# Performance work log

Measured on AMD Instinct MI355X. Metric: run time of the kernel, lower is better.

Reference implementation:

```python
import jax, jax.numpy as jnp
import numpy as np
import math

UNIT = 46
KEY_SIZE = 16
MAX_POS = 50
NEG_BIG = 1.0e12


def _rope_tables(max_pos, d):
    pos = np.arange(max_pos, dtype=np.float32)[:, None]
    div = np.exp(np.arange(0, d, 2, dtype=np.float32) * (-math.log(10000.0) / d))
    sin = np.sin(pos * div)  # [P, d/2]
    cos = np.cos(pos * div)  # [P, d/2]
    # matches torch repeat_interleave(2, dim=-1) of the strided sinusoid table
    cos_rep = np.repeat(cos, 2, axis=-1)  # [P, d]
    sin_rep = np.repeat(sin, 2, axis=-1)  # [P, d]
    return jnp.asarray(cos_rep), jnp.asarray(sin_rep)

_COS, _SIN = _rope_tables(MAX_POS, KEY_SIZE)


def _apply_rope(qw):
    # qw: [B, S, d]
    s = qw.shape[-2]
    qw2 = jnp.stack([-qw[..., 1::2], qw[..., ::2]], axis=-1).reshape(qw.shape)
    return qw * _COS[:s] + qw2 * _SIN[:s]


def setup_inputs() -> dict:
    key = jax.random.key(0)
    ks = jax.random.split(key, 8)
    B, S = 32768, 50
    x = jax.random.normal(ks[0], (B, S, UNIT), dtype=jnp.float32)
    mask = jnp.ones((B, S), dtype=jnp.float32)
    d_in = UNIT
    sc = 1.0 / math.sqrt(d_in)
    Wi = jax.random.uniform(ks[1], (2 * UNIT + KEY_SIZE, d_in), minval=-sc, maxval=sc, dtype=jnp.float32)
    bi = jax.random.uniform(ks[2], (2 * UNIT + KEY_SIZE,), minval=-sc, maxval=sc, dtype=jnp.float32)
    Wo = jax.random.uniform(ks[3], (UNIT, UNIT), minval=-sc, maxval=sc, dtype=jnp.float32)
    bo = jax.random.uniform(ks[4], (UNIT,), minval=-sc, maxval=sc, dtype=jnp.float32)
    Wq = jax.random.uniform(ks[5], (1, UNIT), minval=-sc, maxval=sc, dtype=jnp.float32)
    bq = jax.random.uniform(ks[6], (1,), minval=-sc, maxval=sc, dtype=jnp.float32)
    scale_q = jnp.ones((KEY_SIZE,), jnp.float32)
    offset_q = jnp.zeros((KEY_SIZE,), jnp.float32)
    scale_k = jnp.ones((KEY_SIZE,), jnp.float32)
    offset_k = jnp.zeros((KEY_SIZE,), jnp.float32)
    return {"x": x, "mask": mask, "Wi": Wi, "bi": bi, "Wo": Wo, "bo": bo,
            "scale_q": scale_q, "offset_q": offset_q, "scale_k": scale_k,
            "offset_k": offset_k, "Wq": Wq, "bq": bq}


def reference(x, mask, Wi, bi, Wo, bo, scale_q, offset_q, scale_k, offset_k, Wq, bq):
    # x: [B, S, U], mask: [B, S]
    h = jax.nn.silu(jnp.einsum('bsu,ou->bso', x, Wi) + bi)  # [B, S, 2U+K]
    u, v, qk = jnp.split(h, [UNIT, 2 * UNIT], axis=-1)
    q = _apply_rope(qk * scale_q + offset_q)  # [B, S, K]
    k = _apply_rope(qk * scale_k + offset_k)  # [B, S, K]
    A = jnp.einsum('bik,bjk->bij', q, k) / math.sqrt(KEY_SIZE)  # [B, S, S]
    m = mask[:, None, :]
    A = jax.nn.softmax(A * m + (1.0 - m) * (-NEG_BIG), axis=-1)
    # NOTE: original overwrites the gated output with a plain matmul (u unused)
    out = jnp.einsum('bij,bju->biu', A, v)  # [B, S, U]
    out = jnp.einsum('biu,ou->bio', out, Wo) + bo  # [B, S, U]
    prob = (jnp.einsum('bsu,ou->bso', out, Wq) + bq)[..., 0]  # [B, S]
    prob = prob * mask - (1.0 - mask) * NEG_BIG
    prob = jax.nn.softmax(prob, axis=-1)
    return jnp.sum(out * prob[..., None], axis=1)  # [B, U]
```

## Files before the change

kernel.cpp:

```cpp
#include <hip/hip_runtime.h>
#include <math.h>

#define SEQ 50
#define UNITD 46
#define NEGBIG 1000000000000.0f

typedef _Float16 f16;
typedef f16 f16x4 __attribute__((ext_vector_type(4)));
typedef f16 f16x8 __attribute__((ext_vector_type(8)));
typedef float f32x4 __attribute__((ext_vector_type(4)));

__device__ __forceinline__ float rcpf(float x) { return __builtin_amdgcn_rcpf(x); }

#define ARENA 12800
#define QOFF 0
#define KOFF 2560
#define VOFF 6400
#define MOFF 12544

__device__ __forceinline__ int swzP(int row, int colbyte) {
    return row * 128 + (colbyte ^ ((row & 7) << 4));
}
__device__ __forceinline__ int swzV(int row, int colbyte) {
    return VOFF + row * 128 + (colbyte ^ ((row & 7) << 4));
}

__global__ void prep_kernel(const float* __restrict__ Wi,
                            const float* __restrict__ Wo,
                            f16x8* __restrict__ ws)
{
    const int lane = threadIdx.x & 63;
    const int g = lane >> 4, t = lane & 15;
    #pragma unroll
    for (int nt = 0; nt < 4; ++nt) {
        int c = t + 16 * nt; bool cok = c < 62;
        const float* wr = Wi + (size_t)(UNITD + (cok ? c : 0)) * UNITD;
        #pragma unroll
        for (int kt = 0; kt < 2; ++kt) {
            f16x8 f;
            #pragma unroll
            for (int jj = 0; jj < 8; ++jj) {
                int u = 32 * kt + 8 * g + jj;
                f[jj] = (f16)((cok && u < UNITD) ? wr[u] : 0.f);
            }
            ws[(nt * 2 + kt) * 64 + lane] = f;
        }
    }
    #pragma unroll
    for (int mo = 0; mo < 3; ++mo) {
        int o = 16 * mo + t; bool ook = o < UNITD;
        const float* wr = Wo + (size_t)(ook ? o : 0) * UNITD;
        #pragma unroll
        for (int kt = 0; kt < 2; ++kt) {
            f16x8 f;
            #pragma unroll
            for (int jj = 0; jj < 8; ++jj) {
                int u = 32 * kt + 8 * g + jj;
                f[jj] = (f16)((ook && u < UNITD) ? wr[u] : 0.f);
            }
            ws[512 + (mo * 2 + kt) * 64 + lane] = f;
        }
    }
}

__global__ __launch_bounds__(256, 3) void gau_kernel(
    const float* __restrict__ x,
    const float* __restrict__ mask,
    const f16x8* __restrict__ wf,
    const float* __restrict__ bi,
    const float* __restrict__ bo,
    const float* __restrict__ sq,
    const float* __restrict__ oq,
    const float* __restrict__ sk,
    const float* __restrict__ ok,
    const float* __restrict__ Wq,
    const float* __restrict__ bq,
    float* __restrict__ out,
    int Btot)
{
    const int lane = threadIdx.x & 63;
    const int wid  = threadIdx.x >> 6;
    const int b    = blockIdx.x * 4 + wid;
    const int g    = lane >> 4;
    const int t    = lane & 15;

    __shared__ __align__(16) char smem[4 * ARENA];
    char* wa = smem + wid * ARENA;
    float* M = (float*)(wa + MOFF);

    if (b >= Btot) return;

    M[lane] = (lane < SEQ) ? mask[(size_t)b * SEQ + lane] : 0.f;

    f16x8 bfW[4][2];
    float biv[4];
    #pragma unroll
    for (int nt = 0; nt < 4; ++nt) {
        int c = t + 16 * nt;
        biv[nt] = (c < 62) ? bi[UNITD + c] : 0.f;
        #pragma unroll
        for (int kt = 0; kt < 2; ++kt)
            bfW[nt][kt] = wf[(nt * 2 + kt) * 64 + lane];
    }

    f32x4 hB[4][4];
    #pragma unroll
    for (int mt = 0; mt < 4; ++mt)
        #pragma unroll
        for (int nt = 0; nt < 4; ++nt) {
            f32x4 c; c[0] = biv[nt]; c[1] = biv[nt]; c[2] = biv[nt]; c[3] = biv[nt];
            hB[mt][nt] = c;
        }

    const float* xb = x + (size_t)b * (SEQ * UNITD);
    #pragma unroll
    for (int mt = 0; mt < 4; ++mt) {
        int row = 16 * mt + t; if (row > SEQ - 1) row = SEQ - 1;
        const float* xr = xb + row * UNITD;
        #pragma unroll
        for (int kt = 0; kt < 2; ++kt) {
            f16x8 ax;
            #pragma unroll
            for (int jj = 0; jj < 8; jj += 2) {
                int u = 32 * kt + 8 * g + jj;
                float lo = 0.f, hi = 0.f;
                if (u < UNITD) { float2 w = *(const float2*)(xr + u); lo = w.x; hi = w.y; }
                ax[jj] = (f16)lo; ax[jj + 1] = (f16)hi;
            }
            #pragma unroll
            for (int nt = 0; nt < 4; ++nt)
                hB[mt][nt] = __builtin_amdgcn_mfma_f32_16x16x32_f16(ax, bfW[nt][kt], hB[mt][nt], 0, 0, 0);
        }
    }

    float qkv[4][4];
    #pragma unroll
    for (int mt = 0; mt < 4; ++mt) {
        float s2[4], s3[4];
        #pragma unroll
        for (int nt = 0; nt < 4; ++nt) {
            float sl[4];
            #pragma unroll
            for (int r = 0; r < 4; ++r) {
                float h = hB[mt][nt][r];
                sl[r] = h * rcpf(1.f + __expf(-h));
            }
            int ucol = t + 16 * nt;
            if (nt < 3 && ucol < UNITD) {
                f16x4 pv;
                #pragma unroll
                for (int r = 0; r < 4; ++r) pv[r] = (f16)sl[r];
                *(f16x4*)(wa + swzV(ucol, (16 * mt + 4 * g) * 2)) = pv;
            }
            if (nt == 2) { s2[0]=sl[0]; s2[1]=sl[1]; s2[2]=sl[2]; s2[3]=sl[3]; }
            if (nt == 3) { s3[0]=sl[0]; s3[1]=sl[1]; s3[2]=sl[2]; s3[3]=sl[3]; }
        }
        #pragma unroll
        for (int r = 0; r < 4; ++r) qkv[mt][r] = (t >= 14) ? s2[r] : s3[r];
    }

    {
        f16* Q = (f16*)(wa + QOFF);
        f16* K = (f16*)(wa + KOFF);
        int d = (t >= 14) ? (t - 14) : (t + 2);
        float invf = __expf(-(float)(d >> 1) * 1.1512925464970229f);
        float sgn  = (d & 1) ? 1.f : -1.f;
        float sqd = sq[d], oqd = oq[d], skd = sk[d], okd = ok[d];
        #pragma unroll
        for (int mt = 0; mt < 4; ++mt)
            #pragma unroll
            for (int r = 0; r < 4; ++r) {
                int seq = 16 * mt + 4 * g + r;
                float qv = qkv[mt][r] * sqd + oqd;
                float kv = qkv[mt][r] * skd + okd;
                float qp = __shfl_xor(qv, 1);
                float kp = __shfl_xor(kv, 1);
                float sn, cs;
                __sincosf((float)seq * invf, &sn, &cs);
                Q[seq * 20 + d] = (f16)(qv * cs + sgn * qp * sn);
                K[seq * 20 + d] = (f16)(kv * cs + sgn * kp * sn);
            }
    }

    f16x4 ak[4], bq_[4];
    #pragma unroll
    for (int m4 = 0; m4 < 4; ++m4) ak[m4]  = *(f16x4*)(wa + KOFF + (16 * m4 + t) * 40 + 8 * g);
    #pragma unroll
    for (int n4 = 0; n4 < 4; ++n4) bq_[n4] = *(f16x4*)(wa + QOFF + (16 * n4 + t) * 40 + 8 * g);

    f32x4 pT[4][4];
    #pragma unroll
    for (int m4 = 0; m4 < 4; ++m4)
        #pragma unroll
        for (int n4 = 0; n4 < 4; ++n4) {
            f32x4 z; z[0]=0.f; z[1]=0.f; z[2]=0.f; z[3]=0.f;
            pT[m4][n4] = __builtin_amdgcn_mfma_f32_16x16x16f16(ak[m4], bq_[n4], z, 0, 0, 0);
        }

    float mjv[4][4];
    #pragma unroll
    for (int m4 = 0; m4 < 4; ++m4)
        #pragma unroll
        for (int r = 0; r < 4; ++r) mjv[m4][r] = M[16 * m4 + 4 * g + r];

    #pragma unroll
    for (int n4 = 0; n4 < 4; ++n4) {
        float a_[4][4]; float mx = -INFINITY;
        #pragma unroll
        for (int m4 = 0; m4 < 4; ++m4)
            #pragma unroll
            for (int r = 0; r < 4; ++r) {
                float mj = mjv[m4][r];
                float av = pT[m4][n4][r] * 0.25f * mj - (1.f - mj) * NEGBIG;
                a_[m4][r] = av; mx = fmaxf(mx, av);
            }
        mx = fmaxf(mx, __shfl_xor(mx, 16)); mx = fmaxf(mx, __shfl_xor(mx, 32));
        float sm = 0.f;
        #pragma unroll
        for (int m4 = 0; m4 < 4; ++m4)
            #pragma unroll
            for (int r = 0; r < 4; ++r) { float e = __expf(a_[m4][r] - mx); a_[m4][r] = e; sm += e; }
        sm += __shfl_xor(sm, 16); sm += __shfl_xor(sm, 32);
        float inv = rcpf(sm);
        int i = t + 16 * n4;
        if (i < SEQ) {
            #pragma unroll
            for (int m4 = 0; m4 < 4; ++m4) {
                f16x4 pk;
                #pragma unroll
                for (int r = 0; r < 4; ++r) pk[r] = (f16)(a_[m4][r] * inv);
                *(f16x4*)(wa + swzP(i, (16 * m4 + 4 * g) * 2)) = pk;
            }
        }
    }

    f16x8 bv[3][2];
    #pragma unroll
    for (int nt = 0; nt < 3; ++nt)
        #pragma unroll
        for (int kt = 0; kt < 2; ++kt)
            bv[nt][kt] = *(f16x8*)(wa + swzV(t + 16 * nt, (32 * kt + 8 * g) * 2));

    f32x4 oA[4][3];
    #pragma unroll
    for (int mt = 0; mt < 4; ++mt)
        #pragma unroll
        for (int nt = 0; nt < 3; ++nt) { f32x4 z; z[0]=0.f; z[1]=0.f; z[2]=0.f; z[3]=0.f; oA[mt][nt] = z; }

    #pragma unroll
    for (int mt = 0; mt < 4; ++mt) {
        int pr = 16 * mt + t; if (pr > SEQ - 1) pr = SEQ - 1;
        #pragma unroll
        for (int kt = 0; kt < 2; ++kt) {
            f16x8 ap = *(f16x8*)(wa + swzP(pr, (32 * kt + 8 * g) * 2));
            #pragma unroll
            for (int nt = 0; nt < 3; ++nt)
                oA[mt][nt] = __builtin_amdgcn_mfma_f32_16x16x32_f16(ap, bv[nt][kt], oA[mt][nt], 0, 0, 0);
        }
    }

    #pragma unroll
    for (int mt = 0; mt < 4; ++mt)
        #pragma unroll
        for (int nt = 0; nt < 3; ++nt) {
            int u = t + 16 * nt;
            if (u < UNITD) {
                #pragma unroll
                for (int r = 0; r < 4; ++r) {
                    int i = 4 * g + r + 16 * mt;
                    if (i < SEQ)
                        *(f16*)(wa + swzP(i, u * 2)) = (f16)oA[mt][nt][r];
                }
            }
        }

    f16x8 aw[3][2];
    #pragma unroll
    for (int mo = 0; mo < 3; ++mo)
        #pragma unroll
        for (int kt = 0; kt < 2; ++kt)
            aw[mo][kt] = wf[512 + (mo * 2 + kt) * 64 + lane];

    f32x4 o2[3][4];
    #pragma unroll
    for (int mo = 0; mo < 3; ++mo)
        #pragma unroll
        for (int n4 = 0; n4 < 4; ++n4) { f32x4 z; z[0]=0.f; z[1]=0.f; z[2]=0.f; z[3]=0.f; o2[mo][n4] = z; }

    #pragma unroll
    for (int n4 = 0; n4 < 4; ++n4) {
        int br = t + 16 * n4; if (br > SEQ - 1) br = SEQ - 1;
        #pragma unroll
        for (int kt = 0; kt < 2; ++kt) {
            f16x8 bo_ = *(f16x8*)(wa + swzP(br, (32 * kt + 8 * g) * 2));
            #pragma unroll
            for (int mo = 0; mo < 3; ++mo)
                o2[mo][n4] = __builtin_amdgcn_mfma_f32_16x16x32_f16(aw[mo][kt], bo_, o2[mo][n4], 0, 0, 0);
        }
    }

    float bov[3][4], wqv[3][4];
    #pragma unroll
    for (int mo = 0; mo < 3; ++mo)
        #pragma unroll
        for (int r = 0; r < 4; ++r) {
            int o = 16 * mo + 4 * g + r; bool ok2 = (o < UNITD);
            bov[mo][r] = ok2 ? bo[o] : 0.f;
            wqv[mo][r] = ok2 ? Wq[o] : 0.f;
        }
    #pragma unroll
    for (int mo = 0; mo < 3; ++mo)
        #pragma unroll
        for (int n4 = 0; n4 < 4; ++n4)
            #pragma unroll
            for (int r = 0; r < 4; ++r) o2[mo][n4][r] += bov[mo][r];

    float bq0 = bq[0];
    float tv[4]; float mx2 = -INFINITY;
    #pragma unroll
    for (int n4 = 0; n4 < 4; ++n4) {
        float s = 0.f;
        #pragma unroll
        for (int mo = 0; mo < 3; ++mo)
            #pragma unroll
            for (int r = 0; r < 4; ++r) s += o2[mo][n4][r] * wqv[mo][r];
        s += __shfl_xor(s, 16); s += __shfl_xor(s, 32);
        float hq = s + bq0;
        float mi = M[t + 16 * n4];
        tv[n4] = hq * mi - (1.f - mi) * NEGBIG;
        mx2 = fmaxf(mx2, tv[n4]);
    }
    #pragma unroll
    for (int off = 1; off <= 8; off <<= 1) mx2 = fmaxf(mx2, __shfl_xor(mx2, off));
    float sm2 = 0.f;
    #pragma unroll
    for (int n4 = 0; n4 < 4; ++n4) { float e = __expf(tv[n4] - mx2); tv[n4] = e; sm2 += e; }
    #pragma unroll
    for (int off = 1; off <= 8; off <<= 1) sm2 += __shfl_xor(sm2, off);
    float inv2 = rcpf(sm2);

    #pragma unroll
    for (int mo = 0; mo < 3; ++mo) {
        float racc[4];
        #pragma unroll
        for (int r = 0; r < 4; ++r) {
            float a = 0.f;
            #pragma unroll
            for (int n4 = 0; n4 < 4; ++n4) a += o2[mo][n4][r] * tv[n4];
            racc[r] = a;
        }
        #pragma unroll
        for (int off = 1; off <= 8; off <<= 1)
            #pragma unroll
            for (int r = 0; r < 4; ++r) racc[r] += __shfl_xor(racc[r], off);
        if (t == 0) {
            #pragma unroll
            for (int r = 0; r < 4; ++r) {
                int o = 16 * mo + 4 * g + r;
                if (o < UNITD) out[(size_t)b * UNITD + o] = racc[r] * inv2;
            }
        }
    }
}

extern "C" void kernel_launch(void* const* d_in, const int* in_sizes, int n_in,
                              void* d_out, int out_size, void* d_ws, size_t ws_size,
                              hipStream_t stream) {
    const float* x    = (const float*)d_in[0];
    const float* mask = (const float*)d_in[1];
    const float* Wi   = (const float*)d_in[2];
    const float* bi   = (const float*)d_in[3];
    const float* Wo   = (const float*)d_in[4];
    const float* bo   = (const float*)d_in[5];
    const float* sq   = (const float*)d_in[6];
    const float* oq   = (const float*)d_in[7];
    const float* sk   = (const float*)d_in[8];
    const float* ok   = (const float*)d_in[9];
    const float* Wq   = (const float*)d_in[10];
    const float* bq   = (const float*)d_in[11];
    float* outp       = (float*)d_out;

    prep_kernel<<<1, 64, 0, stream>>>(Wi, Wo, (f16x8*)d_ws);

    const int B = in_sizes[0] / (SEQ * UNITD);
    const int blocks = (B + 3) / 4;
    gau_kernel<<<blocks, 256, 0, stream>>>(x, mask, (const f16x8*)d_ws, bi, bo,
                                           sq, oq, sk, ok, Wq, bq, outp, B);
}
```

Baseline: 202.8 us.

## Shrink per-wave LDS arena with padded 104-byte row stride to raise occupancy

Replaces the 128-byte XOR-swizzled row layout for the P and V tiles with an unswizzled 104-byte row stride (52 halves). This shrinks the per-wave LDS arena from 12800 to 10240 bytes, and the launch bound is raised from 3 to 4 blocks per CU. Stores that would fall past the 50-sequence boundary are now skipped. The out-of-range K-columns in the V operand are masked to zero in registers, so the padding rows and columns never need to be zeroed. The aim is more resident waves to hide latency. The cost is possible LDS bank conflicts without the swizzle, plus register pressure from the tighter launch bound.

```diff
diff --git a/kernel.cpp b/kernel.cpp
--- a/kernel.cpp
+++ b/kernel.cpp
@@ -9,21 +9,16 @@
 typedef f16 f16x4 __attribute__((ext_vector_type(4)));
 typedef f16 f16x8 __attribute__((ext_vector_type(8)));
 typedef float f32x4 __attribute__((ext_vector_type(4)));
+typedef unsigned u32x4 __attribute__((ext_vector_type(4)));
 
 __device__ __forceinline__ float rcpf(float x) { return __builtin_amdgcn_rcpf(x); }
 
-#define ARENA 12800
+#define ARENA 10240
 #define QOFF 0
 #define KOFF 2560
-#define VOFF 6400
-#define MOFF 12544
-
-__device__ __forceinline__ int swzP(int row, int colbyte) {
-    return row * 128 + (colbyte ^ ((row & 7) << 4));
-}
-__device__ __forceinline__ int swzV(int row, int colbyte) {
-    return VOFF + row * 128 + (colbyte ^ ((row & 7) << 4));
-}
+#define VOFF 5200
+#define MOFF 9984
+#define PSTR 104
 
 __global__ void prep_kernel(const float* __restrict__ Wi,
                             const float* __restrict__ Wo,
@@ -63,7 +58,7 @@
     }
 }
 
-__global__ __launch_bounds__(256, 3) void gau_kernel(
+__global__ __launch_bounds__(256, 4) void gau_kernel(
     const float* __restrict__ x,
     const float* __restrict__ mask,
     const f16x8* __restrict__ wf,
@@ -146,11 +141,13 @@
                 sl[r] = h * rcpf(1.f + __expf(-h));
             }
             int ucol = t + 16 * nt;
-            if (nt < 3 && ucol < UNITD) {
+            if (nt < 3 && ucol < UNITD && (mt < 3 || g == 0)) {
+                int seqb = 16 * mt + 4 * g;
                 f16x4 pv;
                 #pragma unroll
-                for (int r = 0; r < 4; ++r) pv[r] = (f16)sl[r];
-                *(f16x4*)(wa + swzV(ucol, (16 * mt + 4 * g) * 2)) = pv;
+                for (int r = 0; r < 4; ++r)
+                    pv[r] = (seqb + r < SEQ) ? (f16)sl[r] : (f16)0.f;
+                *(f16x4*)(wa + VOFF + ucol * PSTR + seqb * 2) = pv;
             }
             if (nt == 2) { s2[0]=sl[0]; s2[1]=sl[1]; s2[2]=sl[2]; s2[3]=sl[3]; }
             if (nt == 3) { s3[0]=sl[0]; s3[1]=sl[1]; s3[2]=sl[2]; s3[3]=sl[3]; }
@@ -226,10 +223,11 @@
         if (i < SEQ) {
             #pragma unroll
             for (int m4 = 0; m4 < 4; ++m4) {
+                if (m4 == 3 && g != 0) continue;
                 f16x4 pk;
                 #pragma unroll
                 for (int r = 0; r < 4; ++r) pk[r] = (f16)(a_[m4][r] * inv);
-                *(f16x4*)(wa + swzP(i, (16 * m4 + 4 * g) * 2)) = pk;
+                *(f16x4*)(wa + i * PSTR + (16 * m4 + 4 * g) * 2) = pk;
             }
         }
     }
@@ -238,8 +236,17 @@
     #pragma unroll
     for (int nt = 0; nt < 3; ++nt)
         #pragma unroll
-        for (int kt = 0; kt < 2; ++kt)
-            bv[nt][kt] = *(f16x8*)(wa + swzV(t + 16 * nt, (32 * kt + 8 * g) * 2));
+        for (int kt = 0; kt < 2; ++kt) {
+            f16x8 v = *(f16x8*)(wa + VOFF + (t + 16 * nt) * PSTR + (32 * kt + 8 * g) * 2);
+            if (kt == 1) {
+                u32x4 w = __builtin_bit_cast(u32x4, v);
+                unsigned mlo = (g <= 2) ? 0xFFFFFFFFu : 0u;
+                unsigned mhi = (g <= 1) ? 0xFFFFFFFFu : 0u;
+                w[0] &= mlo; w[1] &= mlo; w[2] &= mhi; w[3] &= mhi;
+                v = __builtin_bit_cast(f16x8, w);
+            }
+            bv[nt][kt] = v;
+        }
 
     f32x4 oA[4][3];
     #pragma unroll
@@ -252,7 +259,7 @@
         int pr = 16 * mt + t; if (pr > SEQ - 1) pr = SEQ - 1;
         #pragma unroll
         for (int kt = 0; kt < 2; ++kt) {
-            f16x8 ap = *(f16x8*)(wa + swzP(pr, (32 * kt + 8 * g) * 2));
+            f16x8 ap = *(f16x8*)(wa + pr * PSTR + (32 * kt + 8 * g) * 2);
             #pragma unroll
             for (int nt = 0; nt < 3; ++nt)
                 oA[mt][nt] = __builtin_amdgcn_mfma_f32_16x16x32_f16(ap, bv[nt][kt], oA[mt][nt], 0, 0, 0);
@@ -269,7 +276,7 @@
                 for (int r = 0; r < 4; ++r) {
                     int i = 4 * g + r + 16 * mt;
                     if (i < SEQ)
-                        *(f16*)(wa + swzP(i, u * 2)) = (f16)oA[mt][nt][r];
+                        *(f16*)(wa + i * PSTR + u * 2) = (f16)oA[mt][nt][r];
                 }
             }
         }
@@ -292,7 +299,7 @@
         int br = t + 16 * n4; if (br > SEQ - 1) br = SEQ - 1;
         #pragma unroll
         for (int kt = 0; kt < 2; ++kt) {
-            f16x8 bo_ = *(f16x8*)(wa + swzP(br, (32 * kt + 8 * g) * 2));
+            f16x8 bo_ = *(f16x8*)(wa + br * PSTR + (32 * kt + 8 * g) * 2);
             #pragma unroll
             for (int mo = 0; mo < 3; ++mo)
                 o2[mo][n4] = __builtin_amdgcn_mfma_f32_16x16x32_f16(aw[mo][kt], bo_, o2[mo][n4], 0, 0, 0);
```

New measurement: 209.0 us. +3.1%, slower.
